# Performance work log

Measured on AMD Instinct MI355X. Metric: run time of the kernel, lower is better.

Reference implementation:

```python
import jax, jax.numpy as jnp
import numpy as np

N_NODES = 100_000
N_EDGES = 1_600_000
F_IN = 32
F_OUT = 32
DIM = 2
K = 5                      # kernel_size per dim (open spline)
KTOT = K ** DIM            # 25 kernel weight matrices
S = 2 ** DIM               # 4 nonzero linear-B-spline basis terms per edge
NEG_SLOPE = 0.2

# offsets over the 2^DIM corners of the spline cell, [S, DIM]
_OFFSETS = np.array([[(s >> d) & 1 for d in range(DIM)] for s in range(S)], dtype=np.int32)
_STRIDES = np.array([K ** d for d in range(DIM)], dtype=np.int32)


def _spline_basis(pseudo):
    """Degree-1 open B-spline basis. pseudo: [E, DIM] in [0,1].
    Returns basis [E, S] and kernel-weight indices widx [E, S]."""
    offsets = jnp.asarray(_OFFSETS)
    strides = jnp.asarray(_STRIDES)
    p = pseudo * (K - 1)                         # open spline scaling
    fl = jnp.floor(p)
    frac = p - fl                                # [E, DIM]
    b = jnp.where(offsets[None] == 0, 1.0 - frac[:, None, :], frac[:, None, :])
    basis = jnp.prod(b, axis=-1)                 # [E, S]
    idx = jnp.clip(fl.astype(jnp.int32)[:, None, :] + offsets[None], 0, K - 1)
    widx = jnp.sum(idx * strides, axis=-1)       # [E, S] in [0, KTOT)
    return basis, widx


def setup_inputs() -> dict:
    key = jax.random.key(0)
    ks = jax.random.split(key, 7)
    x = jax.random.normal(ks[0], (N_NODES, F_IN), dtype=jnp.float32)
    edge_index = jax.random.randint(ks[1], (2, N_EDGES), 0, N_NODES)
    pseudo = jax.random.uniform(ks[2], (N_EDGES, DIM), dtype=jnp.float32)
    bound = 1.0 / np.sqrt(KTOT * F_IN)           # matches reset_parameters uniform(size, ...)
    weight = jax.random.uniform(ks[3], (KTOT, F_IN, F_OUT), jnp.float32, -bound, bound)
    root_weight = jax.random.uniform(ks[4], (F_IN, F_OUT), jnp.float32, -bound, bound)
    att_weight = jax.random.uniform(ks[5], (2 * F_OUT,), jnp.float32, -bound, bound)
    bias = jax.random.uniform(ks[6], (F_OUT,), jnp.float32, -bound, bound)
    return {"x": x, "edge_index": edge_index, "pseudo": pseudo, "weight": weight,
            "root_weight": root_weight, "att_weight": att_weight, "bias": bias}


def reference(x, edge_index, pseudo, weight, root_weight, att_weight, bias):
    row, col = edge_index[0], edge_index[1]      # row = target, col = source
    basis, widx = _spline_basis(pseudo)          # [E,S], [E,S]

    # Precompute x @ W_k for every kernel weight: [N, KTOT, F_OUT]
    xw = jnp.einsum('nf,kfo->nko', x, weight)
    flat = col[:, None] * KTOT + widx            # [E, S] flat (node, kernel) index
    gathered = xw.reshape(-1, F_OUT)[flat]       # [E, S, F_OUT]
    msg = jnp.einsum('es,esf->ef', basis, gathered)  # spline-weighted edge messages

    x_root = x @ root_weight                     # [N, F_OUT]

    # GAT-style attention logits: cat([x_root[row], msg]) . att_weight
    alpha = x_root[row] @ att_weight[:F_OUT] + msg @ att_weight[F_OUT:]
    alpha = jnp.where(alpha > 0, alpha, NEG_SLOPE * alpha)  # leaky relu

    # segment softmax over incoming edges of each target node
    amax = jax.ops.segment_max(alpha, row, num_segments=N_NODES)
    amax = jnp.where(jnp.isfinite(amax), amax, 0.0)
    ex = jnp.exp(alpha - amax[row])
    denom = jax.ops.segment_sum(ex, row, num_segments=N_NODES)
    att = ex / (denom[row] + 1e-16)

    out = jax.ops.segment_sum(msg * att[:, None], row, num_segments=N_NODES)
    return out + x_root + bias
```

## Files before the change

### kernel.cpp

```cpp
#include <hip/hip_runtime.h>
#include <stdint.h>

#define N_NODES 100000
#define N_EDGES 1600000
#define NBLK_SCAN 391

typedef __attribute__((ext_vector_type(8))) short short8;
typedef __attribute__((ext_vector_type(4))) float float4v;

__device__ __forceinline__ unsigned short f32_to_bf16(float f) {
  uint32_t u = __float_as_uint(f);
  u += 0x7fffu + ((u >> 16) & 1u);
  return (unsigned short)(u >> 16);
}
__device__ __forceinline__ float bf16_to_f32(unsigned short h) {
  return __uint_as_float(((uint32_t)h) << 16);
}
__device__ __forceinline__ unsigned pack2bf16(float a, float b) {
  return (unsigned)f32_to_bf16(a) | ((unsigned)f32_to_bf16(b) << 16);
}

__global__ __launch_bounds__(256) void k_zero(
    const float* __restrict__ weight, const float* __restrict__ root_w,
    const float* __restrict__ att_w,
    int* __restrict__ deg, unsigned short* __restrict__ wbf,
    unsigned long long* __restrict__ tilepack, int* __restrict__ tilectr) {
  int tid = threadIdx.x;
  int b = blockIdx.x;
  int i = b * 256 + tid;
  if (i < N_NODES) deg[i] = 0;
  if (i < NBLK_SCAN) tilepack[i] = 0ull;
  if (i == 0) *tilectr = 0;
  if (b < 100) {
    int e = i;
    int km = e >> 10;
    int rem = e & 1023;
    int kk = rem >> 5;
    int fo = rem & 31;
    int t = km * 2 + (fo >> 4);
    int c = fo & 15;
    int q = kk >> 3, j = kk & 7;
    wbf[((t * 4 + q) * 16 + c) * 8 + j] = f32_to_bf16(weight[e]);
  } else if (b == 100) {
    for (int idx = tid; idx < 1024; idx += 256) {
      int kk = idx >> 5;
      int fo = idx & 31;
      int t = 50 + (fo >> 4);
      int c = fo & 15;
      int q = kk >> 3, j = kk & 7;
      wbf[((t * 4 + q) * 16 + c) * 8 + j] = f32_to_bf16(root_w[idx]);
    }
  } else if (b == 101) {
    for (int idx = tid; idx < 1024; idx += 256) {
      int cg = idx >> 5;
      int kk = idx & 31;
      float s = 0.f;
      if (cg < 25) {
        const float* wp = weight + (cg * 32 + kk) * 32;
#pragma unroll
        for (int fo = 0; fo < 32; fo++) s += wp[fo] * att_w[32 + fo];
      } else if (cg == 25) {
        const float* rp = root_w + kk * 32;
#pragma unroll
        for (int fo = 0; fo < 32; fo++) s += rp[fo] * att_w[fo];
      }
      int t = 52 + (cg >> 4);
      int c = cg & 15;
      int q = kk >> 3, j = kk & 7;
      wbf[((t * 4 + q) * 16 + c) * 8 + j] = f32_to_bf16(s);
    }
  }
}

__global__ __launch_bounds__(256) void k1_xw(
    const float* __restrict__ x, const unsigned short* __restrict__ wbf,
    const int* __restrict__ ei, const float* __restrict__ bias,
    int* __restrict__ deg, unsigned short* __restrict__ rank,
    unsigned short* __restrict__ xw, float* __restrict__ out,
    unsigned short* __restrict__ ydot) {
  __shared__ __align__(16) unsigned short ot[16 * 808];
  int tid = threadIdx.x;
  int b = blockIdx.x;

  int e = b * 256 + tid;
  int rk = atomicAdd(&deg[ei[e]], 1);

  int wave = tid >> 6, lane = tid & 63;
  int quad = lane >> 4, c16 = lane & 15;
  int n0 = b * 16;
  int node = n0 + c16;
  const float* xp = x + (size_t)node * 32 + quad * 8;
  float4 a0 = *reinterpret_cast<const float4*>(xp);
  float4 a1 = *reinterpret_cast<const float4*>(xp + 4);
  short8 xf;
  xf[0] = (short)f32_to_bf16(a0.x); xf[1] = (short)f32_to_bf16(a0.y);
  xf[2] = (short)f32_to_bf16(a0.z); xf[3] = (short)f32_to_bf16(a0.w);
  xf[4] = (short)f32_to_bf16(a1.x); xf[5] = (short)f32_to_bf16(a1.y);
  xf[6] = (short)f32_to_bf16(a1.z); xf[7] = (short)f32_to_bf16(a1.w);

  unsigned short* otn = ot + c16 * 808;
  for (int t = wave; t < 54; t += 4) {
    short8 wf = *reinterpret_cast<const short8*>(wbf + ((t * 4 + quad) * 16 + c16) * 8);
    float4v acc = {0.f, 0.f, 0.f, 0.f};
    acc = __builtin_amdgcn_mfma_f32_16x16x32_bf16(wf, xf, acc, 0, 0, 0);
    if (t < 50) {
      int col = (t >> 1) * 32 + (t & 1) * 16 + quad * 4;
      uint2 pk;
      pk.x = pack2bf16(acc[0], acc[1]);
      pk.y = pack2bf16(acc[2], acc[3]);
      *reinterpret_cast<uint2*>(otn + col) = pk;
    } else if (t < 52) {
      int f0 = (t - 50) * 16 + quad * 4;
      float4 o;
      o.x = acc[0] + bias[f0];
      o.y = acc[1] + bias[f0 + 1];
      o.z = acc[2] + bias[f0 + 2];
      o.w = acc[3] + bias[f0 + 3];
      *reinterpret_cast<float4*>(out + (size_t)node * 32 + f0) = o;
    } else {
      int cg0 = (t - 52) * 16 + quad * 4;
      uint2 pk;
      pk.x = pack2bf16(acc[0], acc[1]);
      pk.y = pack2bf16(acc[2], acc[3]);
      *reinterpret_cast<uint2*>(ydot + (size_t)node * 32 + cg0) = pk;
    }
  }
  __syncthreads();

  const uint4* src = (const uint4*)ot;
  uint4* dst = (uint4*)(xw + (size_t)n0 * 800);
  for (int i = tid; i < 1600; i += 256) {
    int r = i / 100;
    int c = i - r * 100;
    dst[r * 100 + c] = src[r * 101 + c];
  }
  rank[e] = (unsigned short)rk;
}

__global__ __launch_bounds__(256) void k_scan(
    const int* __restrict__ deg, int* __restrict__ offs,
    int* __restrict__ tilectr, unsigned long long* __restrict__ tilepack) {
  __shared__ int s[256];
  __shared__ int sh_tile, sh_excl;
  int tid = threadIdx.x;
  if (tid == 0) sh_tile = atomicAdd(tilectr, 1);
  __syncthreads();
  int tile = sh_tile;
  int i = tile * 256 + tid;
  int v = (i < N_NODES) ? deg[i] : 0;
  s[tid] = v;
  __syncthreads();
  for (int d = 1; d < 256; d <<= 1) {
    int t = (tid >= d) ? s[tid - d] : 0;
    __syncthreads();
    s[tid] += t;
    __syncthreads();
  }
  int incl = s[tid];
  int agg = s[255];
  if (tid == 0) {
    unsigned long long init = ((tile == 0) ? (2ull << 32) : (1ull << 32)) | (unsigned int)agg;
    __hip_atomic_store(&tilepack[tile], init, __ATOMIC_RELEASE, __HIP_MEMORY_SCOPE_AGENT);
    if (tile == 0) sh_excl = 0;
  }
  if (tile > 0 && tid < 64) {
    int excl = 0;
    int base = tile - 1;
    while (true) {
      int look = base - tid;
      unsigned long long pk;
      if (look >= 0) {
        do {
          pk = __hip_atomic_load(&tilepack[look], __ATOMIC_ACQUIRE, __HIP_MEMORY_SCOPE_AGENT);
        } while ((pk >> 32) == 0);
      } else {
        pk = (2ull << 32);
      }
      unsigned long long m2 = __ballot((pk >> 32) == 2);
      int lim = (m2 == 0ull) ? 64 : (__ffsll(m2) - 1);
      int val = (tid <= lim) ? (int)(unsigned int)pk : 0;
#pragma unroll
      for (int m = 1; m < 64; m <<= 1) val += __shfl_xor(val, m);
      excl += val;
      if (lim < 64) break;
      base -= 64;
    }
    if (tid == 0) {
      __hip_atomic_store(&tilepack[tile], (2ull << 32) | (unsigned int)(excl + agg),
                         __ATOMIC_RELEASE, __HIP_MEMORY_SCOPE_AGENT);
      sh_excl = excl;
    }
  }
  __syncthreads();
  if (i < N_NODES) offs[i] = sh_excl + incl - v;
  if (i == N_NODES - 1) offs[N_NODES] = N_EDGES;
}

__global__ __launch_bounds__(256) void kscatter(
    const int* __restrict__ ei, const float* __restrict__ pseudo,
    const int* __restrict__ offs, const unsigned short* __restrict__ rank,
    const unsigned short* __restrict__ ydot, uint2* __restrict__ epack) {
  int e = blockIdx.x * 256 + threadIdx.x;
  int r = ei[e];
  int c = ei[N_EDGES + e];
  int pos = offs[r] + (int)rank[e];
  float p0 = pseudo[2 * e] * 4.f;
  float p1 = pseudo[2 * e + 1] * 4.f;
  float fl0 = floorf(p0), fl1 = floorf(p1);
  float fr0 = p0 - fl0, fr1 = p1 - fl1;
  int i0 = (int)fl0, i1 = (int)fl1;
  int j0p = min(i0 + 1, 4);
  int j1 = 5 * i1, j1p = 5 * min(i1 + 1, 4);
  int rb = c * 32;
  float y0 = bf16_to_f32(ydot[rb + i0 + j1]);
  float y1 = bf16_to_f32(ydot[rb + j0p + j1]);
  float y2 = bf16_to_f32(ydot[rb + i0 + j1p]);
  float y3 = bf16_to_f32(ydot[rb + j0p + j1p]);
  float rd = bf16_to_f32(ydot[(size_t)r * 32 + 25]);
  float fm0 = 1.f - fr0, fm1 = 1.f - fr1;
  float b0 = fm0 * fm1, b1 = fr0 * fm1, b2 = fm0 * fr1, b3 = fr0 * fr1;
  float alpha = rd + b0 * y0 + b1 * y1 + b2 * y2 + b3 * y3;
  alpha = fmaxf(alpha, 0.2f * alpha);
  float ex = __expf(alpha);
  unsigned u = __float_as_uint(ex);
  unsigned exb = (u + 0x7fffu + ((u >> 16) & 1u)) & 0xffff0000u;
  unsigned q0 = __float2uint_rn(fr0 * 255.f);
  unsigned q1 = __float2uint_rn(fr1 * 255.f);
  uint2 pk;
  pk.x = (unsigned)c | ((unsigned)i0 << 17) | ((unsigned)i1 << 20) | (q0 << 23);
  pk.y = exb | q1;
  epack[pos] = pk;
}

__device__ __forceinline__ void edge_step(uint2 pk, const unsigned short* __restrict__ xwf,
                                          float& acc, float& den) {
  int c  = (int)(pk.x & 0x1FFFF);
  int i0 = (int)((pk.x >> 17) & 7);
  int i1 = (int)((pk.x >> 20) & 7);
  float fr0 = (float)((pk.x >> 23) & 255u) * (1.f / 255.f);
  float fr1 = (float)(pk.y & 255u) * (1.f / 255.f);
  float ex = __uint_as_float(pk.y & 0xffff0000u);
  int j0p = min(i0 + 1, 4);
  int j1 = 5 * i1, j1p = 5 * min(i1 + 1, 4);
  int base = c * 800;
  float g0 = bf16_to_f32(xwf[base + (i0 + j1) * 32]);
  float g1 = bf16_to_f32(xwf[base + (j0p + j1) * 32]);
  float g2 = bf16_to_f32(xwf[base + (i0 + j1p) * 32]);
  float g3 = bf16_to_f32(xwf[base + (j0p + j1p) * 32]);
  float fm0 = 1.f - fr0, fm1 = 1.f - fr1;
  float msg = fm1 * (fm0 * g0 + fr0 * g1) + fr1 * (fm0 * g2 + fr0 * g3);
  acc = fmaf(msg, ex, acc);
  den += ex;
}

__global__ __launch_bounds__(256) void k2_csr(
    const int* __restrict__ offs, const uint2* __restrict__ epack,
    const unsigned short* __restrict__ xw, float* __restrict__ out) {
  int tid = threadIdx.x;
  int wave = tid >> 6, lane = tid & 63;
  int node = blockIdx.x * 4 + wave;
  if (node >= N_NODES) return;
  int f = lane & 31, half = lane >> 5;
  int s0 = offs[node], s1 = offs[node + 1];
  const unsigned short* xwf = xw + f;
  float acc = 0.f, den = 0.f;
  int i = s0 + half;

  for (; i + 6 < s1; i += 8) {
    uint2 p0 = epack[i];
    uint2 p1 = epack[i + 2];
    uint2 p2 = epack[i + 4];
    uint2 p3 = epack[i + 6];
    edge_step(p0, xwf, acc, den);
    edge_step(p1, xwf, acc, den);
    edge_step(p2, xwf, acc, den);
    edge_step(p3, xwf, acc, den);
  }
  for (; i < s1; i += 2) edge_step(epack[i], xwf, acc, den);

  acc += __shfl_xor(acc, 32);
  den += __shfl_xor(den, 32);
  if (half == 0) out[node * 32 + f] += acc / (den + 1e-16f);
}

extern "C" void kernel_launch(void* const* d_in, const int* in_sizes, int n_in,
                              void* d_out, int out_size, void* d_ws, size_t ws_size,
                              hipStream_t stream) {
  const float* x      = (const float*)d_in[0];
  const int*   ei     = (const int*)d_in[1];
  const float* pseudo = (const float*)d_in[2];
  const float* weight = (const float*)d_in[3];
  const float* root_w = (const float*)d_in[4];
  const float* att_w  = (const float*)d_in[5];
  const float* bias   = (const float*)d_in[6];
  float* out = (float*)d_out;

  char* ws = (char*)d_ws;
  unsigned short* xw   = (unsigned short*)ws;
  unsigned short* wbf  = (unsigned short*)(ws + 160000000);
  int* deg             = (int*)(ws + 160057344);
  int* offs            = (int*)(ws + 160457344);
  unsigned long long* tilepack = (unsigned long long*)(ws + 160857360);
  int* tilectr         = (int*)(ws + 160860488);
  unsigned short* rank = (unsigned short*)(ws + 160860496);
  unsigned short* ydot = (unsigned short*)(ws + 164060496);
  uint2* epack         = (uint2*)(ws + 170460496);

  hipLaunchKernelGGL(k_zero, dim3(NBLK_SCAN), dim3(256), 0, stream,
                     weight, root_w, att_w, deg, wbf, tilepack, tilectr);
  hipLaunchKernelGGL(k1_xw, dim3(6250), dim3(256), 0, stream,
                     x, wbf, ei, bias, deg, rank, xw, out, ydot);
  hipLaunchKernelGGL(k_scan, dim3(NBLK_SCAN), dim3(256), 0, stream,
                     deg, offs, tilectr, tilepack);
  hipLaunchKernelGGL(kscatter, dim3(6250), dim3(256), 0, stream,
                     ei, pseudo, offs, rank, ydot, epack);
  hipLaunchKernelGGL(k2_csr, dim3(25000), dim3(256), 0, stream,
                     offs, epack, xw, out);
}
```

Baseline: 361.3 us.

## Quantize per-node xW table to int8 and precompute gather offsets per edge

The per-node x@W_k table is stored as int8 with a per-node scale instead of bf16, halving the bytes written in k1 and gathered in the CSR aggregation. The scale is folded into the edge weight in the scatter kernel. The edge record grows to 16 bytes and carries a precomputed base offset plus boundary flags, which removes index arithmetic from the inner loop. Int8 quantization adds precision loss against the reference, and the wider edge record adds epack traffic.

```diff
diff --git a/kernel.cpp b/kernel.cpp
--- a/kernel.cpp
+++ b/kernel.cpp
@@ -18,6 +18,16 @@
 }
 __device__ __forceinline__ unsigned pack2bf16(float a, float b) {
   return (unsigned)f32_to_bf16(a) | ((unsigned)f32_to_bf16(b) << 16);
+}
+__device__ __forceinline__ unsigned bf16hi(float v) {
+  unsigned u = __float_as_uint(v);
+  return (u + 0x7fffu + ((u >> 16) & 1u)) & 0xffff0000u;
+}
+__device__ __forceinline__ void q2(unsigned u, float inv, int& a, int& b) {
+  float lo = __uint_as_float(u << 16);
+  float hi = __uint_as_float(u & 0xffff0000u);
+  a = __float2int_rn(lo * inv);
+  b = __float2int_rn(hi * inv);
 }
 
 __global__ __launch_bounds__(256) void k_zero(
@@ -76,9 +86,10 @@
     const float* __restrict__ x, const unsigned short* __restrict__ wbf,
     const int* __restrict__ ei, const float* __restrict__ bias,
     int* __restrict__ deg, unsigned short* __restrict__ rank,
-    unsigned short* __restrict__ xw, float* __restrict__ out,
-    unsigned short* __restrict__ ydot) {
+    int8_t* __restrict__ xq, float* __restrict__ scale,
+    float* __restrict__ out, unsigned short* __restrict__ ydot) {
   __shared__ __align__(16) unsigned short ot[16 * 808];
+  __shared__ float sinv[16];
   int tid = threadIdx.x;
   int b = blockIdx.x;
 
@@ -127,12 +138,41 @@
   }
   __syncthreads();
 
-  const uint4* src = (const uint4*)ot;
-  uint4* dst = (uint4*)(xw + (size_t)n0 * 800);
+  int nn = tid >> 4, part = tid & 15;
+  const uint4* rowp = (const uint4*)(ot + nn * 808);
+  unsigned mx = 0;
+  for (int j = part; j < 100; j += 16) {
+    uint4 v = rowp[j];
+    unsigned a;
+    a = v.x & 0x7fff7fffu; mx = max(mx, max(a & 0xffffu, a >> 16));
+    a = v.y & 0x7fff7fffu; mx = max(mx, max(a & 0xffffu, a >> 16));
+    a = v.z & 0x7fff7fffu; mx = max(mx, max(a & 0xffffu, a >> 16));
+    a = v.w & 0x7fff7fffu; mx = max(mx, max(a & 0xffffu, a >> 16));
+  }
+#pragma unroll
+  for (int m = 1; m < 16; m <<= 1) mx = max(mx, (unsigned)__shfl_xor((int)mx, m));
+  float s = bf16_to_f32((unsigned short)mx);
+  float inv = (s > 0.f) ? 127.f / s : 0.f;
+  if (part == 0) {
+    sinv[nn] = inv;
+    scale[n0 + nn] = s * (1.f / 127.f);
+  }
+  __syncthreads();
+
   for (int i = tid; i < 1600; i += 256) {
     int r = i / 100;
     int c = i - r * 100;
-    dst[r * 100 + c] = src[r * 101 + c];
+    uint4 v = ((const uint4*)ot)[r * 101 + c];
+    float iv = sinv[r];
+    int b0, b1, b2, b3, b4, b5, b6, b7;
+    q2(v.x, iv, b0, b1); q2(v.y, iv, b2, b3);
+    q2(v.z, iv, b4, b5); q2(v.w, iv, b6, b7);
+    uint2 o;
+    o.x = (unsigned)(b0 & 255) | ((unsigned)(b1 & 255) << 8) |
+          ((unsigned)(b2 & 255) << 16) | ((unsigned)(b3 & 255) << 24);
+    o.y = (unsigned)(b4 & 255) | ((unsigned)(b5 & 255) << 8) |
+          ((unsigned)(b6 & 255) << 16) | ((unsigned)(b7 & 255) << 24);
+    *reinterpret_cast<uint2*>(xq + (size_t)(n0 + r) * 800 + c * 8) = o;
   }
   rank[e] = (unsigned short)rk;
 }
@@ -199,7 +239,8 @@
 __global__ __launch_bounds__(256) void kscatter(
     const int* __restrict__ ei, const float* __restrict__ pseudo,
     const int* __restrict__ offs, const unsigned short* __restrict__ rank,
-    const unsigned short* __restrict__ ydot, uint2* __restrict__ epack) {
+    const unsigned short* __restrict__ ydot, const float* __restrict__ scale,
+    uint4* __restrict__ epack) {
   int e = blockIdx.x * 256 + threadIdx.x;
   int r = ei[e];
   int c = ei[N_EDGES + e];
@@ -222,61 +263,60 @@
   float alpha = rd + b0 * y0 + b1 * y1 + b2 * y2 + b3 * y3;
   alpha = fmaxf(alpha, 0.2f * alpha);
   float ex = __expf(alpha);
-  unsigned u = __float_as_uint(ex);
-  unsigned exb = (u + 0x7fffu + ((u >> 16) & 1u)) & 0xffff0000u;
+  float sex = scale[c] * ex;
   unsigned q0 = __float2uint_rn(fr0 * 255.f);
   unsigned q1 = __float2uint_rn(fr1 * 255.f);
-  uint2 pk;
-  pk.x = (unsigned)c | ((unsigned)i0 << 17) | ((unsigned)i1 << 20) | (q0 << 23);
-  pk.y = exb | q1;
+  uint4 pk;
+  pk.x = q0 | (q1 << 8) | ((i0 < 4 ? 1u : 0u) << 16) | ((i1 < 4 ? 1u : 0u) << 17);
+  pk.y = bf16hi(ex);
+  pk.z = bf16hi(sex);
+  pk.w = (unsigned)c * 800u + (unsigned)(i0 + 5 * i1) * 32u;
   epack[pos] = pk;
 }
 
-__device__ __forceinline__ void edge_step(uint2 pk, const unsigned short* __restrict__ xwf,
+__device__ __forceinline__ void edge_step(uint4 pk, const int8_t* __restrict__ xqf,
                                           float& acc, float& den) {
-  int c  = (int)(pk.x & 0x1FFFF);
-  int i0 = (int)((pk.x >> 17) & 7);
-  int i1 = (int)((pk.x >> 20) & 7);
-  float fr0 = (float)((pk.x >> 23) & 255u) * (1.f / 255.f);
-  float fr1 = (float)(pk.y & 255u) * (1.f / 255.f);
-  float ex = __uint_as_float(pk.y & 0xffff0000u);
-  int j0p = min(i0 + 1, 4);
-  int j1 = 5 * i1, j1p = 5 * min(i1 + 1, 4);
-  int base = c * 800;
-  float g0 = bf16_to_f32(xwf[base + (i0 + j1) * 32]);
-  float g1 = bf16_to_f32(xwf[base + (j0p + j1) * 32]);
-  float g2 = bf16_to_f32(xwf[base + (i0 + j1p) * 32]);
-  float g3 = bf16_to_f32(xwf[base + (j0p + j1p) * 32]);
+  float fr0 = (float)(pk.x & 255u) * (1.f / 255.f);
+  float fr1 = (float)((pk.x >> 8) & 255u) * (1.f / 255.f);
+  int d0 = (pk.x & 0x10000u) ? 32 : 0;
+  int d1 = (pk.x & 0x20000u) ? 160 : 0;
+  float ex = __uint_as_float(pk.y);
+  float sex = __uint_as_float(pk.z);
+  const int8_t* p = xqf + pk.w;
+  float g0 = (float)p[0];
+  float g1 = (float)p[d0];
+  float g2 = (float)p[d1];
+  float g3 = (float)p[d0 + d1];
   float fm0 = 1.f - fr0, fm1 = 1.f - fr1;
   float msg = fm1 * (fm0 * g0 + fr0 * g1) + fr1 * (fm0 * g2 + fr0 * g3);
-  acc = fmaf(msg, ex, acc);
+  acc = fmaf(msg, sex, acc);
   den += ex;
 }
 
 __global__ __launch_bounds__(256) void k2_csr(
-    const int* __restrict__ offs, const uint2* __restrict__ epack,
-    const unsigned short* __restrict__ xw, float* __restrict__ out) {
+    const int* __restrict__ offs, const uint4* __restrict__ epack,
+    const int8_t* __restrict__ xq, float* __restrict__ out) {
   int tid = threadIdx.x;
   int wave = tid >> 6, lane = tid & 63;
   int node = blockIdx.x * 4 + wave;
   if (node >= N_NODES) return;
   int f = lane & 31, half = lane >> 5;
   int s0 = offs[node], s1 = offs[node + 1];
-  const unsigned short* xwf = xw + f;
+  const int8_t* xqf = xq + f;
   float acc = 0.f, den = 0.f;
   int i = s0 + half;
 
   for (; i + 6 < s1; i += 8) {
-    uint2 p0 = epack[i];
-    uint2 p1 = epack[i + 2];
-    uint2 p2 = epack[i + 4];
-    uint2 p3 = epack[i + 6];
-    edge_step(p0, xwf, acc, den);
-    edge_step(p1, xwf, acc, den);
-    edge_step(p2, xwf, acc, den);
-    edge_step(p3, xwf, acc, den);
-  }
-  for (; i < s1; i += 2) edge_step(epack[i], xwf, acc, den);
+    uint4 p0 = epack[i];
+    uint4 p1 = epack[i + 2];
+    uint4 p2 = epack[i + 4];
+    uint4 p3 = epack[i + 6];
+    edge_step(p0, xqf, acc, den);
+    edge_step(p1, xqf, acc, den);
+    edge_step(p2, xqf, acc, den);
+    edge_step(p3, xqf, acc, den);
+  }
+  for (; i < s1; i += 2) edge_step(epack[i], xqf, acc, den);
 
   acc += __shfl_xor(acc, 32);
   den += __shfl_xor(den, 32);
@@ -296,24 +336,25 @@
   float* out = (float*)d_out;
 
   char* ws = (char*)d_ws;
-  unsigned short* xw   = (unsigned short*)ws;
-  unsigned short* wbf  = (unsigned short*)(ws + 160000000);
-  int* deg             = (int*)(ws + 160057344);
-  int* offs            = (int*)(ws + 160457344);
-  unsigned long long* tilepack = (unsigned long long*)(ws + 160857360);
-  int* tilectr         = (int*)(ws + 160860488);
-  unsigned short* rank = (unsigned short*)(ws + 160860496);
-  unsigned short* ydot = (unsigned short*)(ws + 164060496);
-  uint2* epack         = (uint2*)(ws + 170460496);
+  int8_t* xq          = (int8_t*)ws;
+  float* scale        = (float*)(ws + 80000000);
+  unsigned short* wbf = (unsigned short*)(ws + 80400000);
+  int* deg            = (int*)(ws + 80457344);
+  int* offs           = (int*)(ws + 80857344);
+  unsigned long long* tilepack = (unsigned long long*)(ws + 81257360);
+  int* tilectr        = (int*)(ws + 81260488);
+  unsigned short* rank = (unsigned short*)(ws + 81260496);
+  unsigned short* ydot = (unsigned short*)(ws + 84460496);
+  uint4* epack        = (uint4*)(ws + 90860496);
 
   hipLaunchKernelGGL(k_zero, dim3(NBLK_SCAN), dim3(256), 0, stream,
                      weight, root_w, att_w, deg, wbf, tilepack, tilectr);
   hipLaunchKernelGGL(k1_xw, dim3(6250), dim3(256), 0, stream,
-                     x, wbf, ei, bias, deg, rank, xw, out, ydot);
+                     x, wbf, ei, bias, deg, rank, xq, scale, out, ydot);
   hipLaunchKernelGGL(k_scan, dim3(NBLK_SCAN), dim3(256), 0, stream,
                      deg, offs, tilectr, tilepack);
   hipLaunchKernelGGL(kscatter, dim3(6250), dim3(256), 0, stream,
-                     ei, pseudo, offs, rank, ydot, epack);
+                     ei, pseudo, offs, rank, ydot, scale, epack);
   hipLaunchKernelGGL(k2_csr, dim3(25000), dim3(256), 0, stream,
-                     offs, epack, xw, out);
-}
+                     offs, epack, xq, out);
+}
```

After: 353.6 us. 2.1% less time.
